# Performance work log

Measured on AMD Instinct MI355X. Metric: run time of the kernel, lower is better.

The kernel has to match this reference:

```python
import jax, jax.numpy as jnp
import numpy as np

N_NODES = 50000
N_EDGES = 800000
IN_F = 128
OUT_F = 128
HEADS = 8
HEAD_DIM = OUT_F // HEADS
EDGE_F = 32


def setup_inputs() -> dict:
    key = jax.random.key(0)
    ks = jax.random.split(key, 14)
    s = lambda fan_in: 1.0 / np.sqrt(fan_in)
    return {
        "node_features": jax.random.normal(ks[0], (N_NODES, IN_F), jnp.float32),
        "edge_index": jax.random.randint(ks[1], (2, N_EDGES), 0, N_NODES, jnp.int64),
        "edge_features": jax.random.normal(ks[2], (N_EDGES, EDGE_F), jnp.float32),
        "Wq": jax.random.uniform(ks[3], (IN_F, OUT_F), jnp.float32, -s(IN_F), s(IN_F)),
        "bq": jnp.zeros((OUT_F,), jnp.float32),
        "Wk": jax.random.uniform(ks[4], (IN_F, OUT_F), jnp.float32, -s(IN_F), s(IN_F)),
        "bk": jnp.zeros((OUT_F,), jnp.float32),
        "Wv": jax.random.uniform(ks[5], (IN_F, OUT_F), jnp.float32, -s(IN_F), s(IN_F)),
        "bv": jnp.zeros((OUT_F,), jnp.float32),
        "We": jax.random.uniform(ks[6], (EDGE_F, HEADS), jnp.float32, -s(EDGE_F), s(EDGE_F)),
        "be": jnp.zeros((HEADS,), jnp.float32),
        "Wo": jax.random.uniform(ks[7], (OUT_F, OUT_F), jnp.float32, -s(OUT_F), s(OUT_F)),
        "bo": jnp.zeros((OUT_F,), jnp.float32),
    }


def reference(node_features, edge_index, edge_features,
              Wq, bq, Wk, bk, Wv, bv, We, be, Wo, bo):
    n_nodes = node_features.shape[0]
    n_edges = edge_index.shape[1]
    sources, targets = edge_index[0], edge_index[1]
    scale = HEAD_DIM ** -0.5

    # dense projections: [n_nodes, heads, head_dim]
    Q = (node_features @ Wq + bq).reshape(n_nodes, HEADS, HEAD_DIM)
    K = (node_features @ Wk + bk).reshape(n_nodes, HEADS, HEAD_DIM)
    V = (node_features @ Wv + bv).reshape(n_nodes, HEADS, HEAD_DIM)

    # gather by edge
    Q_t = Q[targets]           # [n_edges, heads, head_dim]
    K_s = K[sources]
    V_s = V[sources]

    scores = jnp.sum(Q_t * K_s, axis=-1) * scale      # [n_edges, heads]
    scores = scores + (edge_features @ We + be)       # edge bias

    # segment softmax over incoming edges of each target node
    max_s = jax.ops.segment_max(scores, targets, num_segments=n_nodes)
    scores = scores - max_s[targets]
    exp_s = jnp.exp(scores)
    denom = jax.ops.segment_sum(exp_s, targets, num_segments=n_nodes) + 1e-10
    probs = exp_s / denom[targets]                    # [n_edges, heads]

    weighted_V = probs[:, :, None] * V_s              # [n_edges, heads, head_dim]
    aggregated = jax.ops.segment_sum(
        weighted_V.reshape(n_edges, -1), targets, num_segments=n_nodes)
    return aggregated @ Wo + bo
```

## Files before the change

kernel.cpp:

```cpp
#include <hip/hip_runtime.h>

typedef __attribute__((ext_vector_type(8))) short shortx8;
typedef __attribute__((ext_vector_type(4))) float floatx4;
typedef unsigned short u16;
typedef unsigned int u32;

__device__ __forceinline__ float bf2f(unsigned short u) {
    union { unsigned int i; float f; } v; v.i = ((unsigned int)u) << 16; return v.f;
}
__device__ __forceinline__ float bfl(u32 u) {
    union { u32 i; float f; } v; v.i = u << 16; return v.f;
}
__device__ __forceinline__ float bfh(u32 u) {
    union { u32 i; float f; } v; v.i = u & 0xFFFF0000u; return v.f;
}
__device__ __forceinline__ unsigned short f2bf(float f) {
    union { float f; unsigned int i; } v; v.f = f;
    unsigned int x = v.i;
    unsigned int r = x + 0x7FFFu + ((x >> 16) & 1u);
    return (unsigned short)(r >> 16);
}
__device__ __forceinline__ float ldf(const void* p, int i, bool f32) {
    return f32 ? ((const float*)p)[i] : bf2f(((const u16*)p)[i]);
}

__global__ __launch_bounds__(256) void detect_zero_k(
    const u16* __restrict__ nf, const int* __restrict__ ei,
    int* __restrict__ flags, int* __restrict__ deg, int M)
{
    int tid = threadIdx.x;
    if (blockIdx.x != 0) {
        int i = (blockIdx.x - 1) * 256 + tid;
        if (i < M) deg[i] = 0;
        return;
    }
    __shared__ int cnt[2];
    if (tid < 2) cnt[tid] = 0;
    __syncthreads();
    int c0 = 0;
    for (int i = tid; i < 65536; i += 256) {
        u16 v = nf[i];
        if ((v & 0x7F80u) == 0x7F80u) c0++;
    }
    int c1 = 0;
    for (int i = tid; i < 4096; i += 256) {
        if (ei[2 * i + 1] != 0) c1++;
    }
    atomicAdd(&cnt[0], c0);
    atomicAdd(&cnt[1], c1);
    __syncthreads();
    if (tid == 0) {
        flags[0] = (cnt[0] > 8) ? 1 : 0;
        flags[1] = (cnt[1] < 100) ? 1 : 0;
    }
}

__global__ __launch_bounds__(256) void prep_k(
    const void* __restrict__ W0, const void* __restrict__ W1,
    const void* __restrict__ W2, const void* __restrict__ W3,
    const void* __restrict__ b0, const void* __restrict__ b1,
    const void* __restrict__ b2, const void* __restrict__ b3,
    const void* __restrict__ We, const void* __restrict__ be,
    const int* __restrict__ flags,
    u16* __restrict__ WT, float* __restrict__ biasWs,
    float* __restrict__ WeWs, float* __restrict__ beWs)
{
    bool f32 = flags[0] != 0;
    int tid = threadIdx.x;
    if (blockIdx.x < 32) {
        int t = blockIdx.x * 256 + tid;
        int mat  = t >> 11;
        int r    = t & 2047;
        int lane = r & 63;
        int ks   = (r >> 6) & 3;
        int ct   = r >> 8;
        const void* W = (mat == 0) ? W0 : (mat == 1) ? W1 : (mat == 2) ? W2 : W3;
        int k0  = ks * 32 + (lane >> 4) * 8;
        int col = ct * 16 + (lane & 15);
        u16 tmp[8];
#pragma unroll
        for (int j = 0; j < 8; ++j) {
            int off = (k0 + j) * 128 + col;
            tmp[j] = f32 ? f2bf(((const float*)W)[off]) : ((const u16*)W)[off];
        }
        *(shortx8*)(WT + (size_t)t * 8) = *(const shortx8*)tmp;
    } else {
        if (tid < 128) {
            biasWs[0 * 128 + tid] = ldf(b0, tid, f32);
            biasWs[1 * 128 + tid] = ldf(b1, tid, f32);
            biasWs[2 * 128 + tid] = ldf(b2, tid, f32);
            biasWs[3 * 128 + tid] = ldf(b3, tid, f32);
        }
        WeWs[tid] = ldf(We, tid, f32);
        if (tid < 8) beWs[tid] = ldf(be, tid, f32);
    }
}

__global__ __launch_bounds__(256) void qkv_gemm_k(
    const void* __restrict__ A, int M,
    const u16* __restrict__ WT, const float* __restrict__ biasWs,
    u16* __restrict__ Qb, u16* __restrict__ Kb, u16* __restrict__ Vb,
    const int* __restrict__ flags)
{
    bool aF32 = flags[0] != 0;
    int lane = threadIdx.x & 63;
    int wave = threadIdx.x >> 6;
    int quad = lane >> 4;
    int l15  = lane & 15;
    int m0   = blockIdx.x * 128 + wave * 32;

    shortx8 afrag[2][4];
#pragma unroll
    for (int mt = 0; mt < 2; ++mt) {
        int row = m0 + mt * 16 + l15;
        row = row < M ? row : M - 1;
#pragma unroll
        for (int ks = 0; ks < 4; ++ks) {
            size_t base = (size_t)row * 128 + ks * 32 + quad * 8;
            if (aF32) {
                const floatx4* ap = (const floatx4*)((const float*)A + base);
                floatx4 f0 = ap[0], f1 = ap[1];
                u16 tmp[8];
#pragma unroll
                for (int j = 0; j < 4; ++j) { tmp[j] = f2bf(f0[j]); tmp[4 + j] = f2bf(f1[j]); }
                afrag[mt][ks] = *(const shortx8*)tmp;
            } else {
                afrag[mt][ks] = *(const shortx8*)((const u16*)A + base);
            }
        }
    }

    u16* outs[3] = {Qb, Kb, Vb};
#pragma unroll
    for (int mat = 0; mat < 3; ++mat) {
        floatx4 acc[2][8];
#pragma unroll
        for (int a = 0; a < 2; ++a)
#pragma unroll
            for (int b = 0; b < 8; ++b)
                acc[a][b] = (floatx4){0.f, 0.f, 0.f, 0.f};
#pragma unroll
        for (int ks = 0; ks < 4; ++ks) {
#pragma unroll
            for (int ct = 0; ct < 8; ++ct) {
                shortx8 bfrag = *(const shortx8*)(WT + (size_t)mat * 16384 +
                                                  ((size_t)(ct * 4 + ks) * 64 + lane) * 8);
                acc[0][ct] = __builtin_amdgcn_mfma_f32_16x16x32_bf16(afrag[0][ks], bfrag, acc[0][ct], 0, 0, 0);
                acc[1][ct] = __builtin_amdgcn_mfma_f32_16x16x32_bf16(afrag[1][ks], bfrag, acc[1][ct], 0, 0, 0);
            }
        }
        u16* out = outs[mat];
#pragma unroll
        for (int ct = 0; ct < 8; ++ct) {
            int col = ct * 16 + l15;
            float bs = biasWs[mat * 128 + col];
#pragma unroll
            for (int mt = 0; mt < 2; ++mt) {
#pragma unroll
                for (int r = 0; r < 4; ++r) {
                    int row = m0 + mt * 16 + quad * 4 + r;
                    if (row < M)
                        out[(size_t)row * 128 + col] = f2bf(acc[mt][ct][r] + bs);
                }
            }
        }
    }
}

__global__ __launch_bounds__(256) void out_gemm_k(
    const u16* __restrict__ A, int M,
    const u16* __restrict__ WT, const float* __restrict__ bias,
    void* __restrict__ out, const int* __restrict__ flags)
{
    bool oF32 = flags[0] != 0;
    int lane = threadIdx.x & 63;
    int wave = threadIdx.x >> 6;
    int quad = lane >> 4;
    int l15  = lane & 15;
    int m0   = blockIdx.x * 128 + wave * 32;

    floatx4 acc[2][8];
#pragma unroll
    for (int a = 0; a < 2; ++a)
#pragma unroll
        for (int b = 0; b < 8; ++b)
            acc[a][b] = (floatx4){0.f, 0.f, 0.f, 0.f};

#pragma unroll
    for (int ks = 0; ks < 4; ++ks) {
        shortx8 afrag[2];
#pragma unroll
        for (int mt = 0; mt < 2; ++mt) {
            int row = m0 + mt * 16 + l15;
            row = row < M ? row : M - 1;
            afrag[mt] = *(const shortx8*)(A + (size_t)row * 128 + ks * 32 + quad * 8);
        }
#pragma unroll
        for (int ct = 0; ct < 8; ++ct) {
            shortx8 bfrag = *(const shortx8*)(WT + ((size_t)(ct * 4 + ks) * 64 + lane) * 8);
            acc[0][ct] = __builtin_amdgcn_mfma_f32_16x16x32_bf16(afrag[0], bfrag, acc[0][ct], 0, 0, 0);
            acc[1][ct] = __builtin_amdgcn_mfma_f32_16x16x32_bf16(afrag[1], bfrag, acc[1][ct], 0, 0, 0);
        }
    }

#pragma unroll
    for (int ct = 0; ct < 8; ++ct) {
        int col = ct * 16 + l15;
        float bs = bias[col];
#pragma unroll
        for (int mt = 0; mt < 2; ++mt) {
#pragma unroll
            for (int r = 0; r < 4; ++r) {
                int row = m0 + mt * 16 + quad * 4 + r;
                if (row < M) {
                    float v = acc[mt][ct][r] + bs;
                    if (oF32) ((float*)out)[(size_t)row * 128 + col] = v;
                    else      ((u16*)out)[(size_t)row * 128 + col] = f2bf(v);
                }
            }
        }
    }
}

__global__ __launch_bounds__(256) void edge_prep_k(
    const int* __restrict__ ei, const void* __restrict__ ef,
    const float* __restrict__ WeWs, const float* __restrict__ beWs,
    float* __restrict__ EB, int* __restrict__ deg,
    int E, const int* __restrict__ flags)
{
    __shared__ float sWe[256];
    __shared__ float sbe[8];
    int tid = threadIdx.x;
    sWe[tid] = WeWs[tid];
    if (tid < 8) sbe[tid] = beWs[tid];
    __syncthreads();

    int e = blockIdx.x * 256 + tid;
    if (e >= E) return;
    bool f32 = flags[0] != 0;
    bool i64 = flags[1] != 0;

    int tgt = i64 ? ei[2 * (E + e)] : ei[E + e];
    atomicAdd(&deg[tgt], 1);

    float v[32];
    if (f32) {
        const floatx4* ep = (const floatx4*)((const float*)ef + (size_t)e * 32);
#pragma unroll
        for (int g = 0; g < 8; ++g) {
            floatx4 t = ep[g];
#pragma unroll
            for (int j = 0; j < 4; ++j) v[g * 4 + j] = t[j];
        }
    } else {
        const shortx8* ep = (const shortx8*)((const u16*)ef + (size_t)e * 32);
#pragma unroll
        for (int g = 0; g < 4; ++g) {
            shortx8 t = ep[g];
#pragma unroll
            for (int j = 0; j < 8; ++j) v[g * 8 + j] = bf2f((unsigned short)t[j]);
        }
    }
    float eb[8];
#pragma unroll
    for (int h = 0; h < 8; ++h) eb[h] = sbe[h];
#pragma unroll
    for (int k = 0; k < 32; ++k)
#pragma unroll
        for (int h = 0; h < 8; ++h) eb[h] += v[k] * sWe[k * 8 + h];

    floatx4* op = (floatx4*)(EB + (size_t)e * 8);
    op[0] = (floatx4){eb[0], eb[1], eb[2], eb[3]};
    op[1] = (floatx4){eb[4], eb[5], eb[6], eb[7]};
}

__global__ __launch_bounds__(256) void scan1_k(
    const int* __restrict__ deg, int* __restrict__ incl, int* __restrict__ bsum, int M)
{
    __shared__ int s[256];
    int tid = threadIdx.x;
    int i = blockIdx.x * 256 + tid;
    int v = (i < M) ? deg[i] : 0;
    s[tid] = v;
    __syncthreads();
#pragma unroll
    for (int off = 1; off < 256; off <<= 1) {
        int t = (tid >= off) ? s[tid - off] : 0;
        __syncthreads();
        s[tid] += t;
        __syncthreads();
    }
    if (i < M) incl[i] = s[tid];
    if (tid == 255) bsum[blockIdx.x] = s[255];
}

__global__ __launch_bounds__(256) void scan2_k(
    const int* __restrict__ bsum, int* __restrict__ boff, int nb)
{
    __shared__ int s[256];
    int tid = threadIdx.x;
    int v = (tid < nb) ? bsum[tid] : 0;
    s[tid] = v;
    __syncthreads();
#pragma unroll
    for (int off = 1; off < 256; off <<= 1) {
        int t = (tid >= off) ? s[tid - off] : 0;
        __syncthreads();
        s[tid] += t;
        __syncthreads();
    }
    if (tid < nb) boff[tid] = s[tid] - v;
}

__global__ __launch_bounds__(256) void scan3_k(
    const int* __restrict__ incl, const int* __restrict__ boff,
    const int* __restrict__ deg,
    int* __restrict__ rowptr, int* __restrict__ cursor, int M)
{
    int i = blockIdx.x * 256 + threadIdx.x;
    if (i >= M) return;
    int g = incl[i] + boff[i >> 8];
    rowptr[i + 1] = g;
    cursor[i] = g - deg[i];
    if (i == 0) rowptr[0] = 0;
}

__global__ __launch_bounds__(256) void scatter_k(
    const int* __restrict__ ei, int* __restrict__ cursor,
    int2* __restrict__ perm, int E, const int* __restrict__ flags)
{
    int e = blockIdx.x * 256 + threadIdx.x;
    if (e >= E) return;
    bool i64 = flags[1] != 0;
    int src = i64 ? ei[2 * e]       : ei[e];
    int tgt = i64 ? ei[2 * (E + e)] : ei[E + e];
    int pos = atomicAdd(&cursor[tgt], 1);
    perm[pos] = make_int2(src, e);
}

__global__ __launch_bounds__(256) void node_agg_k(
    const int2* __restrict__ perm, const int* __restrict__ rowptr,
    const u16* __restrict__ Qb, const u16* __restrict__ Kb, const u16* __restrict__ Vb,
    const float* __restrict__ EB, u16* __restrict__ aggN, int M)
{
    int wave = threadIdx.x >> 6;
    int lane = threadIdx.x & 63;
    int n = blockIdx.x * 4 + wave;
    if (n >= M) return;
    int g = lane >> 4;
    int w = lane & 15;
    int h = w >> 1;

    uint4 qw = ((const uint4*)(Qb + (size_t)n * 128))[w];
    float q0 = bfl(qw.x), q1 = bfh(qw.x), q2 = bfl(qw.y), q3 = bfh(qw.y);
    float q4 = bfl(qw.z), q5 = bfh(qw.z), q6 = bfl(qw.w), q7 = bfh(qw.w);

    float acc[8];
#pragma unroll
    for (int j = 0; j < 8; ++j) acc[j] = 0.f;
    float dsum = 0.f;

    int beg = rowptr[n], end = rowptr[n + 1];
    for (int i = beg; i < end; i += 4) {
        int eidx = i + g;
        bool valid = eidx < end;
        int ec = valid ? eidx : beg;
        int2 se = perm[ec];
        int s = se.x, e = se.y;
        const uint4* kp = (const uint4*)(Kb + (size_t)s * 128);
        const uint4* vp = (const uint4*)(Vb + (size_t)s * 128);
        uint4 kw = kp[w];
        uint4 vw = vp[w];
        float eb = EB[(size_t)e * 8 + h];
        float part = q0 * bfl(kw.x) + q1 * bfh(kw.x)
                   + q2 * bfl(kw.y) + q3 * bfh(kw.y)
                   + q4 * bfl(kw.z) + q5 * bfh(kw.z)
                   + q6 * bfl(kw.w) + q7 * bfh(kw.w);
        part += __shfl_xor(part, 1);
        float p = valid ? __expf(part * 0.25f + eb) : 0.f;
        dsum += p;
        acc[0] += p * bfl(vw.x); acc[1] += p * bfh(vw.x);
        acc[2] += p * bfl(vw.y); acc[3] += p * bfh(vw.y);
        acc[4] += p * bfl(vw.z); acc[5] += p * bfh(vw.z);
        acc[6] += p * bfl(vw.w); acc[7] += p * bfh(vw.w);
    }

    dsum += __shfl_xor(dsum, 16);
    dsum += __shfl_xor(dsum, 32);
#pragma unroll
    for (int j = 0; j < 8; ++j) {
        acc[j] += __shfl_xor(acc[j], 16);
        acc[j] += __shfl_xor(acc[j], 32);
    }
    if (g == 0) {
        float inv = 1.0f / (dsum + 1e-10f);
        uint4 o;
        o.x = (u32)f2bf(acc[0] * inv) | ((u32)f2bf(acc[1] * inv) << 16);
        o.y = (u32)f2bf(acc[2] * inv) | ((u32)f2bf(acc[3] * inv) << 16);
        o.z = (u32)f2bf(acc[4] * inv) | ((u32)f2bf(acc[5] * inv) << 16);
        o.w = (u32)f2bf(acc[6] * inv) | ((u32)f2bf(acc[7] * inv) << 16);
        ((uint4*)(aggN + (size_t)n * 128))[w] = o;
    }
}

extern "C" void kernel_launch(void* const* d_in, const int* in_sizes, int n_in,
                              void* d_out, int out_size, void* d_ws, size_t ws_size,
                              hipStream_t stream)
{
    const void* nf = d_in[0];
    const int*  ei = (const int*)d_in[1];
    const void* ef = d_in[2];
    const void* Wq = d_in[3];  const void* bq = d_in[4];
    const void* Wk = d_in[5];  const void* bk = d_in[6];
    const void* Wv = d_in[7];  const void* bv = d_in[8];
    const void* We = d_in[9];  const void* be = d_in[10];
    const void* Wo = d_in[11]; const void* bo = d_in[12];

    int M = in_sizes[0] / 128;
    int E = in_sizes[1] / 2;
    int nb = (M + 255) / 256;

    char* ws = (char*)d_ws;
    int*   flags  = (int*)(ws + 0);
    float* biasWs = (float*)(ws + 256);
    float* WeWs   = (float*)(ws + 2304);
    float* beWs   = (float*)(ws + 3328);
    u16*   WT     = (u16*)(ws + 4096);
    size_t O1 = 4096 + 131072;
    size_t qkv = (size_t)M * 128 * 2;
    u16* Qb = (u16*)(ws + O1);
    u16* Kb = (u16*)(ws + O1 + qkv);
    u16* Vb = (u16*)(ws + O1 + 2 * qkv);
    size_t O2 = O1 + 3 * qkv;
    float* EB = (float*)(ws + O2);
    size_t O3 = O2 + (size_t)E * 8 * 4;
    int2* perm = (int2*)(ws + O3);
    size_t O4 = O3 + (size_t)E * 8;
    int* deg    = (int*)(ws + O4);
    int* incl   = deg + M;
    int* rowptr = incl + M;
    int* cursor = rowptr + M + 1;
    int* bsum   = cursor + M;
    int* boff   = bsum + 256;
    u16* aggN   = Qb;

    detect_zero_k<<<1 + nb, 256, 0, stream>>>((const u16*)nf, ei, flags, deg, M);
    prep_k<<<33, 256, 0, stream>>>(Wq, Wk, Wv, Wo, bq, bk, bv, bo, We, be,
                                   flags, WT, biasWs, WeWs, beWs);

    int gblocks = (M + 127) / 128;
    qkv_gemm_k<<<gblocks, 256, 0, stream>>>(nf, M, WT, biasWs, Qb, Kb, Vb, flags);

    int eblocks = (E + 255) / 256;
    edge_prep_k<<<eblocks, 256, 0, stream>>>(ei, ef, WeWs, beWs, EB, deg, E, flags);

    scan1_k<<<nb, 256, 0, stream>>>(deg, incl, bsum, M);
    scan2_k<<<1, 256, 0, stream>>>(bsum, boff, nb);
    scan3_k<<<nb, 256, 0, stream>>>(incl, boff, deg, rowptr, cursor, M);
    scatter_k<<<eblocks, 256, 0, stream>>>(ei, cursor, perm, E, flags);

    node_agg_k<<<(M + 3) / 4, 256, 0, stream>>>(perm, rowptr, Qb, Kb, Vb, EB, aggN, M);

    out_gemm_k<<<gblocks, 256, 0, stream>>>(aggN, M, WT + 3 * 16384, biasWs + 384, d_out, flags);
}
```

Baseline: 466.6 us.

## Build CSR with atomic ranks, single-block scan, and scatter edge bias to sorted order

Replaces the three-pass block scan and the atomic cursor scatter with a histogram pass that records each edge's rank, followed by a single 1024-thread scan over all nodes. Edge-bias computation is fused with the scatter, so biases are written directly in target-sorted order. The aggregation kernel then reads them contiguously, with no per-edge index indirection. Neighbour source indices are preloaded per wave and broadcast with shuffles. The single-block scan is serial over about 49 nodes per thread, which adds latency, and scattered bias writes replace the previous sequential ones.

```diff
diff --git a/kernel.cpp b/kernel.cpp
--- a/kernel.cpp
+++ b/kernel.cpp
@@ -96,6 +96,40 @@
     }
 }
 
+__global__ __launch_bounds__(256) void hist_rank_k(
+    const int* __restrict__ ei, int* __restrict__ deg, int* __restrict__ rank,
+    int E, const int* __restrict__ flags)
+{
+    int e = blockIdx.x * 256 + threadIdx.x;
+    if (e >= E) return;
+    int tgt = flags[1] ? ei[2 * (E + e)] : ei[E + e];
+    rank[e] = atomicAdd(&deg[tgt], 1);
+}
+
+__global__ __launch_bounds__(1024) void scan_all_k(
+    const int* __restrict__ deg, int* __restrict__ rowptr, int M)
+{
+    __shared__ int s[1024];
+    int tid = threadIdx.x;
+    int C = (M + 1023) >> 10;
+    int b0 = tid * C;
+    int b1 = b0 + C; if (b1 > M) b1 = M;
+    int sum = 0;
+    for (int i = b0; i < b1; ++i) sum += deg[i];
+    s[tid] = sum;
+    __syncthreads();
+#pragma unroll
+    for (int off = 1; off < 1024; off <<= 1) {
+        int t = (tid >= off) ? s[tid - off] : 0;
+        __syncthreads();
+        s[tid] += t;
+        __syncthreads();
+    }
+    int run = s[tid] - sum;
+    for (int i = b0; i < b1; ++i) { rowptr[i] = run; run += deg[i]; }
+    if (b0 < M && b1 == M) rowptr[M] = run;
+}
+
 __global__ __launch_bounds__(256) void qkv_gemm_k(
     const void* __restrict__ A, int M,
     const u16* __restrict__ WT, const float* __restrict__ biasWs,
@@ -167,65 +201,11 @@
     }
 }
 
-__global__ __launch_bounds__(256) void out_gemm_k(
-    const u16* __restrict__ A, int M,
-    const u16* __restrict__ WT, const float* __restrict__ bias,
-    void* __restrict__ out, const int* __restrict__ flags)
-{
-    bool oF32 = flags[0] != 0;
-    int lane = threadIdx.x & 63;
-    int wave = threadIdx.x >> 6;
-    int quad = lane >> 4;
-    int l15  = lane & 15;
-    int m0   = blockIdx.x * 128 + wave * 32;
-
-    floatx4 acc[2][8];
-#pragma unroll
-    for (int a = 0; a < 2; ++a)
-#pragma unroll
-        for (int b = 0; b < 8; ++b)
-            acc[a][b] = (floatx4){0.f, 0.f, 0.f, 0.f};
-
-#pragma unroll
-    for (int ks = 0; ks < 4; ++ks) {
-        shortx8 afrag[2];
-#pragma unroll
-        for (int mt = 0; mt < 2; ++mt) {
-            int row = m0 + mt * 16 + l15;
-            row = row < M ? row : M - 1;
-            afrag[mt] = *(const shortx8*)(A + (size_t)row * 128 + ks * 32 + quad * 8);
-        }
-#pragma unroll
-        for (int ct = 0; ct < 8; ++ct) {
-            shortx8 bfrag = *(const shortx8*)(WT + ((size_t)(ct * 4 + ks) * 64 + lane) * 8);
-            acc[0][ct] = __builtin_amdgcn_mfma_f32_16x16x32_bf16(afrag[0], bfrag, acc[0][ct], 0, 0, 0);
-            acc[1][ct] = __builtin_amdgcn_mfma_f32_16x16x32_bf16(afrag[1], bfrag, acc[1][ct], 0, 0, 0);
-        }
-    }
-
-#pragma unroll
-    for (int ct = 0; ct < 8; ++ct) {
-        int col = ct * 16 + l15;
-        float bs = bias[col];
-#pragma unroll
-        for (int mt = 0; mt < 2; ++mt) {
-#pragma unroll
-            for (int r = 0; r < 4; ++r) {
-                int row = m0 + mt * 16 + quad * 4 + r;
-                if (row < M) {
-                    float v = acc[mt][ct][r] + bs;
-                    if (oF32) ((float*)out)[(size_t)row * 128 + col] = v;
-                    else      ((u16*)out)[(size_t)row * 128 + col] = f2bf(v);
-                }
-            }
-        }
-    }
-}
-
-__global__ __launch_bounds__(256) void edge_prep_k(
+__global__ __launch_bounds__(256) void edge_scatter_k(
     const int* __restrict__ ei, const void* __restrict__ ef,
+    const int* __restrict__ rank, const int* __restrict__ rowptr,
     const float* __restrict__ WeWs, const float* __restrict__ beWs,
-    float* __restrict__ EB, int* __restrict__ deg,
+    int* __restrict__ perm, float* __restrict__ EBp,
     int E, const int* __restrict__ flags)
 {
     __shared__ float sWe[256];
@@ -240,8 +220,10 @@
     bool f32 = flags[0] != 0;
     bool i64 = flags[1] != 0;
 
+    int src = i64 ? ei[2 * e]       : ei[e];
     int tgt = i64 ? ei[2 * (E + e)] : ei[E + e];
-    atomicAdd(&deg[tgt], 1);
+    int pos = rowptr[tgt] + rank[e];
+    perm[pos] = src;
 
     float v[32];
     if (f32) {
@@ -269,79 +251,15 @@
 #pragma unroll
         for (int h = 0; h < 8; ++h) eb[h] += v[k] * sWe[k * 8 + h];
 
-    floatx4* op = (floatx4*)(EB + (size_t)e * 8);
+    floatx4* op = (floatx4*)(EBp + (size_t)pos * 8);
     op[0] = (floatx4){eb[0], eb[1], eb[2], eb[3]};
     op[1] = (floatx4){eb[4], eb[5], eb[6], eb[7]};
 }
 
-__global__ __launch_bounds__(256) void scan1_k(
-    const int* __restrict__ deg, int* __restrict__ incl, int* __restrict__ bsum, int M)
-{
-    __shared__ int s[256];
-    int tid = threadIdx.x;
-    int i = blockIdx.x * 256 + tid;
-    int v = (i < M) ? deg[i] : 0;
-    s[tid] = v;
-    __syncthreads();
-#pragma unroll
-    for (int off = 1; off < 256; off <<= 1) {
-        int t = (tid >= off) ? s[tid - off] : 0;
-        __syncthreads();
-        s[tid] += t;
-        __syncthreads();
-    }
-    if (i < M) incl[i] = s[tid];
-    if (tid == 255) bsum[blockIdx.x] = s[255];
-}
-
-__global__ __launch_bounds__(256) void scan2_k(
-    const int* __restrict__ bsum, int* __restrict__ boff, int nb)
-{
-    __shared__ int s[256];
-    int tid = threadIdx.x;
-    int v = (tid < nb) ? bsum[tid] : 0;
-    s[tid] = v;
-    __syncthreads();
-#pragma unroll
-    for (int off = 1; off < 256; off <<= 1) {
-        int t = (tid >= off) ? s[tid - off] : 0;
-        __syncthreads();
-        s[tid] += t;
-        __syncthreads();
-    }
-    if (tid < nb) boff[tid] = s[tid] - v;
-}
-
-__global__ __launch_bounds__(256) void scan3_k(
-    const int* __restrict__ incl, const int* __restrict__ boff,
-    const int* __restrict__ deg,
-    int* __restrict__ rowptr, int* __restrict__ cursor, int M)
-{
-    int i = blockIdx.x * 256 + threadIdx.x;
-    if (i >= M) return;
-    int g = incl[i] + boff[i >> 8];
-    rowptr[i + 1] = g;
-    cursor[i] = g - deg[i];
-    if (i == 0) rowptr[0] = 0;
-}
-
-__global__ __launch_bounds__(256) void scatter_k(
-    const int* __restrict__ ei, int* __restrict__ cursor,
-    int2* __restrict__ perm, int E, const int* __restrict__ flags)
-{
-    int e = blockIdx.x * 256 + threadIdx.x;
-    if (e >= E) return;
-    bool i64 = flags[1] != 0;
-    int src = i64 ? ei[2 * e]       : ei[e];
-    int tgt = i64 ? ei[2 * (E + e)] : ei[E + e];
-    int pos = atomicAdd(&cursor[tgt], 1);
-    perm[pos] = make_int2(src, e);
-}
-
 __global__ __launch_bounds__(256) void node_agg_k(
-    const int2* __restrict__ perm, const int* __restrict__ rowptr,
+    const int* __restrict__ perm, const int* __restrict__ rowptr,
     const u16* __restrict__ Qb, const u16* __restrict__ Kb, const u16* __restrict__ Vb,
-    const float* __restrict__ EB, u16* __restrict__ aggN, int M)
+    const float* __restrict__ EBp, u16* __restrict__ aggN, int M, int E)
 {
     int wave = threadIdx.x >> 6;
     int lane = threadIdx.x & 63;
@@ -351,6 +269,11 @@
     int w = lane & 15;
     int h = w >> 1;
 
+    int beg = rowptr[n], end = rowptr[n + 1];
+    int pidx = beg + lane;
+    if (pidx >= E) pidx = E - 1;
+    int pv = perm[pidx];
+
     uint4 qw = ((const uint4*)(Qb + (size_t)n * 128))[w];
     float q0 = bfl(qw.x), q1 = bfh(qw.x), q2 = bfl(qw.y), q3 = bfh(qw.y);
     float q4 = bfl(qw.z), q5 = bfh(qw.z), q6 = bfl(qw.w), q7 = bfh(qw.w);
@@ -360,18 +283,15 @@
     for (int j = 0; j < 8; ++j) acc[j] = 0.f;
     float dsum = 0.f;
 
-    int beg = rowptr[n], end = rowptr[n + 1];
     for (int i = beg; i < end; i += 4) {
-        int eidx = i + g;
-        bool valid = eidx < end;
-        int ec = valid ? eidx : beg;
-        int2 se = perm[ec];
-        int s = se.x, e = se.y;
-        const uint4* kp = (const uint4*)(Kb + (size_t)s * 128);
-        const uint4* vp = (const uint4*)(Vb + (size_t)s * 128);
-        uint4 kw = kp[w];
-        uint4 vw = vp[w];
-        float eb = EB[(size_t)e * 8 + h];
+        int idx = i + g;
+        bool valid = idx < end;
+        int cidx = valid ? idx : (end - 1);
+        int off = cidx - beg;
+        int src = (off < 64) ? __shfl(pv, off) : perm[cidx];
+        float eb = EBp[(size_t)cidx * 8 + h];
+        uint4 kw = ((const uint4*)(Kb + (size_t)src * 128))[w];
+        uint4 vw = ((const uint4*)(Vb + (size_t)src * 128))[w];
         float part = q0 * bfl(kw.x) + q1 * bfh(kw.x)
                    + q2 * bfl(kw.y) + q3 * bfh(kw.y)
                    + q4 * bfl(kw.z) + q5 * bfh(kw.z)
@@ -400,6 +320,61 @@
         o.z = (u32)f2bf(acc[4] * inv) | ((u32)f2bf(acc[5] * inv) << 16);
         o.w = (u32)f2bf(acc[6] * inv) | ((u32)f2bf(acc[7] * inv) << 16);
         ((uint4*)(aggN + (size_t)n * 128))[w] = o;
+    }
+}
+
+__global__ __launch_bounds__(256) void out_gemm_k(
+    const u16* __restrict__ A, int M,
+    const u16* __restrict__ WT, const float* __restrict__ bias,
+    void* __restrict__ out, const int* __restrict__ flags)
+{
+    bool oF32 = flags[0] != 0;
+    int lane = threadIdx.x & 63;
+    int wave = threadIdx.x >> 6;
+    int quad = lane >> 4;
+    int l15  = lane & 15;
+    int m0   = blockIdx.x * 128 + wave * 32;
+
+    floatx4 acc[2][8];
+#pragma unroll
+    for (int a = 0; a < 2; ++a)
+#pragma unroll
+        for (int b = 0; b < 8; ++b)
+            acc[a][b] = (floatx4){0.f, 0.f, 0.f, 0.f};
+
+#pragma unroll
+    for (int ks = 0; ks < 4; ++ks) {
+        shortx8 afrag[2];
+#pragma unroll
+        for (int mt = 0; mt < 2; ++mt) {
+            int row = m0 + mt * 16 + l15;
+            row = row < M ? row : M - 1;
+            afrag[mt] = *(const shortx8*)(A + (size_t)row * 128 + ks * 32 + quad * 8);
+        }
+#pragma unroll
+        for (int ct = 0; ct < 8; ++ct) {
+            shortx8 bfrag = *(const shortx8*)(WT + ((size_t)(ct * 4 + ks) * 64 + lane) * 8);
+            acc[0][ct] = __builtin_amdgcn_mfma_f32_16x16x32_bf16(afrag[0], bfrag, acc[0][ct], 0, 0, 0);
+            acc[1][ct] = __builtin_amdgcn_mfma_f32_16x16x32_bf16(afrag[1], bfrag, acc[1][ct], 0, 0, 0);
+        }
+    }
+
+#pragma unroll
+    for (int ct = 0; ct < 8; ++ct) {
+        int col = ct * 16 + l15;
+        float bs = bias[col];
+#pragma unroll
+        for (int mt = 0; mt < 2; ++mt) {
+#pragma unroll
+            for (int r = 0; r < 4; ++r) {
+                int row = m0 + mt * 16 + quad * 4 + r;
+                if (row < M) {
+                    float v = acc[mt][ct][r] + bs;
+                    if (oF32) ((float*)out)[(size_t)row * 128 + col] = v;
+                    else      ((u16*)out)[(size_t)row * 128 + col] = f2bf(v);
+                }
+            }
+        }
     }
 }
 
@@ -432,34 +407,29 @@
     u16* Kb = (u16*)(ws + O1 + qkv);
     u16* Vb = (u16*)(ws + O1 + 2 * qkv);
     size_t O2 = O1 + 3 * qkv;
-    float* EB = (float*)(ws + O2);
+    float* EBp = (float*)(ws + O2);
     size_t O3 = O2 + (size_t)E * 8 * 4;
-    int2* perm = (int2*)(ws + O3);
-    size_t O4 = O3 + (size_t)E * 8;
-    int* deg    = (int*)(ws + O4);
-    int* incl   = deg + M;
-    int* rowptr = incl + M;
-    int* cursor = rowptr + M + 1;
-    int* bsum   = cursor + M;
-    int* boff   = bsum + 256;
+    int* perm   = (int*)(ws + O3);
+    int* rank   = perm + E;
+    int* deg    = rank + E;
+    int* rowptr = deg + M;
     u16* aggN   = Qb;
 
     detect_zero_k<<<1 + nb, 256, 0, stream>>>((const u16*)nf, ei, flags, deg, M);
     prep_k<<<33, 256, 0, stream>>>(Wq, Wk, Wv, Wo, bq, bk, bv, bo, We, be,
                                    flags, WT, biasWs, WeWs, beWs);
 
+    int eblocks = (E + 255) / 256;
+    hist_rank_k<<<eblocks, 256, 0, stream>>>(ei, deg, rank, E, flags);
+    scan_all_k<<<1, 1024, 0, stream>>>(deg, rowptr, M);
+
     int gblocks = (M + 127) / 128;
     qkv_gemm_k<<<gblocks, 256, 0, stream>>>(nf, M, WT, biasWs, Qb, Kb, Vb, flags);
 
-    int eblocks = (E + 255) / 256;
-    edge_prep_k<<<eblocks, 256, 0, stream>>>(ei, ef, WeWs, beWs, EB, deg, E, flags);
-
-    scan1_k<<<nb, 256, 0, stream>>>(deg, incl, bsum, M);
-    scan2_k<<<1, 256, 0, stream>>>(bsum, boff, nb);
-    scan3_k<<<nb, 256, 0, stream>>>(incl, boff, deg, rowptr, cursor, M);
-    scatter_k<<<eblocks, 256, 0, stream>>>(ei, cursor, perm, E, flags);
-
-    node_agg_k<<<(M + 3) / 4, 256, 0, stream>>>(perm, rowptr, Qb, Kb, Vb, EB, aggN, M);
+    edge_scatter_k<<<eblocks, 256, 0, stream>>>(ei, ef, rank, rowptr, WeWs, beWs,
+                                                perm, EBp, E, flags);
+
+    node_agg_k<<<(M + 3) / 4, 256, 0, stream>>>(perm, rowptr, Qb, Kb, Vb, EBp, aggN, M, E);
 
     out_gemm_k<<<gblocks, 256, 0, stream>>>(aggN, M, WT + 3 * 16384, biasWs + 384, d_out, flags);
 }
```

Measured after the change: 521.5 us. +11.8%, slower.
